# Optimization experiments

Hardware: AMD Instinct MI355X
Metric: run time of the kernel (lower is better)

## Reference

```python
import jax, jax.numpy as jnp
import numpy as np
from jax import lax

N, E, G = 20000, 640000, 16
NA, H, NG, L, NC = 21, 128, 50, 6, 97
CUTOFF = 10.0
LOG2 = 0.6931471805599453

def ssp(v):
    # ShiftedSoftplus: softplus(x) - log(2)
    return jax.nn.softplus(v) - LOG2

def setup_inputs() -> dict:
    key = jax.random.key(0)
    ks = jax.random.split(key, 24)
    s = 0.08  # xavier-ish scale for 128-wide layers
    inp = {
        "x": jax.random.normal(ks[0], (N, NA), dtype=jnp.float32),
        "pos": jax.random.uniform(ks[1], (N, 3), dtype=jnp.float32, minval=0.0, maxval=30.0),
        "edge_index": jax.random.randint(ks[2], (2, E), 0, N, dtype=jnp.int64),
        "batch": jnp.sort(jax.random.randint(ks[3], (N,), 0, G, dtype=jnp.int64)),
        # embedding Linear(21 -> 128), weights stored [in, out]
        "emb_w": jax.random.normal(ks[4], (NA, H), dtype=jnp.float32) * 0.15,
        "emb_b": jnp.zeros((H,), dtype=jnp.float32),
        # per-interaction-block params, stacked over L layers
        "mlp1_w": jax.random.normal(ks[5], (L, NG, H), dtype=jnp.float32) * 0.12,
        "mlp1_b": jnp.zeros((L, H), dtype=jnp.float32),
        "mlp2_w": jax.random.normal(ks[6], (L, H, H), dtype=jnp.float32) * s,
        "mlp2_b": jnp.zeros((L, H), dtype=jnp.float32),
        "conv1_w": jax.random.normal(ks[7], (L, H, H), dtype=jnp.float32) * s,  # no bias
        "conv2_w": jax.random.normal(ks[8], (L, H, H), dtype=jnp.float32) * s,
        "conv2_b": jnp.zeros((L, H), dtype=jnp.float32),
        "lin_w": jax.random.normal(ks[9], (L, H, H), dtype=jnp.float32) * s,
        "lin_b": jnp.zeros((L, H), dtype=jnp.float32),
        # head (note: original reuses self.lin1 twice, act is ReLU, dropout eval=identity)
        "lin1_w": jax.random.normal(ks[10], (H, H), dtype=jnp.float32) * s,
        "lin1_b": jnp.zeros((H,), dtype=jnp.float32),
        "lin2_w": jax.random.normal(ks[11], (H, NC), dtype=jnp.float32) * s,
        "lin2_b": jnp.zeros((NC,), dtype=jnp.float32),
    }
    return inp

def reference(x, pos, edge_index, batch, emb_w, emb_b, mlp1_w, mlp1_b, mlp2_w,
              mlp2_b, conv1_w, conv2_w, conv2_b, lin_w, lin_b, lin1_w, lin1_b,
              lin2_w, lin2_b):
    row, col = edge_index[0], edge_index[1]  # source j, target i
    d = pos[row] - pos[col]                  # [E,3]
    edge_weight = jnp.sqrt(jnp.sum(d * d, axis=-1))  # [E]
    # Gaussian smearing
    offset = jnp.linspace(0.0, CUTOFF, NG)
    coeff = -0.5 / (offset[1] - offset[0]) ** 2
    edge_attr = jnp.exp(coeff * (edge_weight[:, None] - offset[None, :]) ** 2)  # [E,NG]
    # cosine cutoff
    C = 0.5 * (jnp.cos(edge_weight * jnp.pi / CUTOFF) + 1.0)  # [E]

    h = x @ emb_w + emb_b  # [N,H]

    def block(h, p):
        m1w, m1b, m2w, m2b, c1w, c2w, c2b, lw, lb = p
        # edge MLP filter times cutoff envelope
        Wf = (ssp(edge_attr @ m1w + m1b) @ m2w + m2b) * C[:, None]  # [E,H]
        hx = h @ c1w                                 # lin1 (no bias)
        msg = hx[row] * Wf                           # gather + modulate
        agg = jax.ops.segment_sum(msg, col, num_segments=N)  # scatter-add
        y = ssp(agg @ c2w + c2b)
        y = y @ lw + lb
        return h + y, None

    h, _ = lax.scan(block, h, (mlp1_w, mlp1_b, mlp2_w, mlp2_b,
                               conv1_w, conv2_w, conv2_b, lin_w, lin_b))

    h = jax.nn.relu(h @ lin1_w + lin1_b)
    # global mean pool
    ones = jnp.ones((N,), dtype=h.dtype)
    counts = jnp.maximum(jax.ops.segment_sum(ones, batch, num_segments=G), 1.0)
    graph_emb = jax.ops.segment_sum(h, batch, num_segments=G) / counts[:, None]  # [G,H]
    h2 = jax.nn.relu(graph_emb @ lin1_w + lin1_b)  # lin1 reused; dropout=identity (eval)
    out = h2 @ lin2_w + lin2_b                     # [G,NC]
    return graph_emb, out
```

## Files before the change

### kernel.cpp

```cpp
#include <hip/hip_runtime.h>
#include <hip/hip_bf16.h>

#define HD 128
#define NGAUSS 50
#define NLAYER 6
#define NGRAPH 16
#define NCLS 97
#define NTAB2 8192
#define WMAX 12.0f

typedef __attribute__((ext_vector_type(8))) short bf16x8;
typedef __attribute__((ext_vector_type(4))) float f32x4;
typedef __attribute__((ext_vector_type(8))) ushort u16x8;
typedef __attribute__((ext_vector_type(4))) ushort u16x4;

__device__ __forceinline__ float ssp_f(float x) {
    float e = __expf(-fabsf(x));
    return fmaxf(x, 0.0f) + __logf(0.5f + 0.5f * e);
}
__device__ __forceinline__ ushort f2bf(float f) {
    uint u = __float_as_uint(f);
    return (ushort)((u + 0x7FFFu + ((u >> 16) & 1u)) >> 16);
}
__device__ __forceinline__ float bf2f(ushort s) {
    return __uint_as_float(((uint)s) << 16);
}

__global__ void hist_kernel(const int* __restrict__ col, int* __restrict__ deg, int E) {
    int e = blockIdx.x * blockDim.x + threadIdx.x;
    if (e < E) atomicAdd(&deg[col[e]], 1);
}

__global__ void scan1_kernel(const int* __restrict__ deg, int* __restrict__ rowp,
                             int* __restrict__ bsum, int N) {
    __shared__ int sm[256];
    const int t = threadIdx.x, i = blockIdx.x * 256 + t;
    int v = (i < N) ? deg[i] : 0;
    sm[t] = v;
    __syncthreads();
    for (int off = 1; off < 256; off <<= 1) {
        int x = sm[t];
        int a = (t >= off) ? sm[t - off] : 0;
        __syncthreads();
        sm[t] = x + a;
        __syncthreads();
    }
    if (i < N) rowp[i] = sm[t] - v;
    if (t == 255) bsum[blockIdx.x] = sm[255];
}
__global__ void scan2_kernel(const int* __restrict__ bsum, int* __restrict__ boff,
                             int NB, int* __restrict__ rowpN) {
    __shared__ int sm[256];
    const int t = threadIdx.x;
    int v = (t < NB) ? bsum[t] : 0;
    sm[t] = v;
    __syncthreads();
    for (int off = 1; off < 256; off <<= 1) {
        int x = sm[t];
        int a = (t >= off) ? sm[t - off] : 0;
        __syncthreads();
        sm[t] = x + a;
        __syncthreads();
    }
    if (t < NB) boff[t] = sm[t] - v;
    if (t == 255) *rowpN = sm[255];
}
__global__ void scan3_kernel(int* __restrict__ rowp, const int* __restrict__ boff,
                             int* __restrict__ cursor, int N) {
    int i = blockIdx.x * blockDim.x + threadIdx.x;
    if (i < N) {
        int r = rowp[i] + boff[i >> 8];
        rowp[i] = r;
        cursor[i] = r;
    }
}

__global__ void fill_kernel(const int* __restrict__ row, const int* __restrict__ col,
                            const float* __restrict__ pos, int* __restrict__ cursor,
                            uint* __restrict__ meta, int E) {
    int e = blockIdx.x * blockDim.x + threadIdx.x;
    if (e >= E) return;
    int c = col[e], r = row[e];
    int slot = atomicAdd(&cursor[c], 1);
    float dx = pos[r*3+0] - pos[c*3+0];
    float dy = pos[r*3+1] - pos[c*3+1];
    float dz = pos[r*3+2] - pos[c*3+2];
    float w = sqrtf(dx*dx + dy*dy + dz*dz);
    const float invDW = (float)(NTAB2 - 1) / WMAX;
    int i = (int)(w * invDW + 0.5f);
    i = min(i, NTAB2 - 1);
    meta[slot] = ((uint)r) | (((uint)i) << 16);
}

__global__ void prep_kernel(const float* __restrict__ m1w, const float* __restrict__ c1w,
                            const float* __restrict__ c2w, const float* __restrict__ lw,
                            const float* __restrict__ l1w, const float* __restrict__ m2w,
                            ushort* __restrict__ m1T, ushort* __restrict__ nodeThi,
                            ushort* __restrict__ nodeTlo, ushort* __restrict__ m2T) {
    int idx = blockIdx.x * blockDim.x + threadIdx.x;
    const int S1 = 6*128*64, S2 = 19*128*128, S3 = 6*128*128;
    if (idx < S1) {
        int l = idx / 8192, r = idx % 8192, c = r / 64, k = r % 64;
        float v = (k < NGAUSS) ? m1w[(size_t)l*NGAUSS*128 + k*128 + c] : 0.0f;
        m1T[(size_t)l*8192 + c*64 + k] = f2bf(v);
    } else if (idx < S1 + S2) {
        int j = idx - S1;
        int m = j / 16384, r = j % 16384, c = r / 128, k = r % 128;
        const float* src;
        if (m < 6)       src = c1w + (size_t)m*16384;
        else if (m < 12) src = c2w + (size_t)(m-6)*16384;
        else if (m < 18) src = lw  + (size_t)(m-12)*16384;
        else             src = l1w;
        float v = src[k*128 + c];
        ushort hi = f2bf(v);
        nodeThi[(size_t)m*16384 + c*128 + k] = hi;
        nodeTlo[(size_t)m*16384 + c*128 + k] = f2bf(v - bf2f(hi));
    } else if (idx < S1 + S2 + S3) {
        int j = idx - S1 - S2;
        int l = j / 16384, r = j % 16384, c = r / 128, k = r % 128;
        m2T[(size_t)l*16384 + c*128 + k] = f2bf(m2w[(size_t)l*16384 + k*128 + c]);
    }
}

__global__ void embed_kernel(const float* __restrict__ x,
                             const float* __restrict__ emb_w, const float* __restrict__ emb_b,
                             float* __restrict__ h, int N) {
    int idx = blockIdx.x * blockDim.x + threadIdx.x;
    if (idx >= N * HD) return;
    int n = idx >> 7, t = idx & 127;
    float acc = emb_b[t];
    #pragma unroll
    for (int a = 0; a < 21; ++a) acc += x[n*21 + a] * emb_w[a*HD + t];
    h[idx] = acc;
}

__global__ __launch_bounds__(256, 2) void buildtab_kernel(
        const ushort* __restrict__ m1T_all, const ushort* __restrict__ m2T_all,
        const float* __restrict__ m1b_all, const float* __restrict__ m2b_all,
        ushort* __restrict__ Tb6) {
    __shared__ ushort A1[128 * 64];
    __shared__ ushort B1[128 * 64];
    __shared__ ushort U [128 * 128];
    __shared__ float CV[128];
    char* A1b = (char*)A1;
    char* B1b = (char*)B1;
    char* Ub  = (char*)U;
    const int tid  = threadIdx.x;
    const int lane = tid & 63;
    const int wave = tid >> 6;
    const int l15  = lane & 15;
    const int kgrp = (lane >> 4) * 8;
    const int rbase = wave * 32;
    const int NTILES = NTAB2 / 128;
    const int layer = blockIdx.x / NTILES;
    const int mt    = blockIdx.x % NTILES;
    const ushort* m1T = m1T_all + (size_t)layer * 8192;
    const ushort* m2T = m2T_all + (size_t)layer * 16384;
    const float*  m1b = m1b_all + layer * HD;
    const float*  m2b = m2b_all + layer * HD;

    const float step = 10.0f / 49.0f;
    const float coeff = -0.5f / (step * step);
    const float DW = WMAX / (float)(NTAB2 - 1);

    #pragma unroll
    for (int p = 0; p < 4; ++p) {
        int rr = p * 32 + (tid >> 3);
        int k8 = (tid & 7) * 8;
        u16x8 v = *reinterpret_cast<const u16x8*>(&m1T[(size_t)rr * 64 + k8]);
        *reinterpret_cast<u16x8*>(&B1b[rr*128 + ((2*k8) ^ ((rr & 7) << 4))]) = v;
    }
    if (tid < 128) {
        float w = (float)(mt*128 + tid) * DW;
        CV[tid] = 0.5f * (__cosf(w * 0.31415926535897931f) + 1.0f);
    }

    float b1c[8], b2c[8];
    #pragma unroll
    for (int cb = 0; cb < 8; ++cb) { b1c[cb] = m1b[cb*16 + l15]; b2c[cb] = m2b[cb*16 + l15]; }

    #pragma unroll
    for (int p = 0; p < 4; ++p) {
        int rr = p * 32 + (tid >> 3);
        int k8 = (tid & 7) * 8;
        float w = (float)(mt*128 + rr) * DW;
        u16x8 v;
        #pragma unroll
        for (int j = 0; j < 8; ++j) {
            int k = k8 + j;
            float d = w - (float)k * step;
            float g = (k < NGAUSS) ? __expf(coeff * d * d) : 0.0f;
            v[j] = f2bf(g);
        }
        *reinterpret_cast<u16x8*>(&A1b[rr*128 + ((2*k8) ^ ((rr & 7) << 4))]) = v;
    }
    __syncthreads();

    f32x4 acc1[2][8];
    #pragma unroll
    for (int i = 0; i < 2; ++i)
        #pragma unroll
        for (int j = 0; j < 8; ++j) { acc1[i][j].x=0.f; acc1[i][j].y=0.f; acc1[i][j].z=0.f; acc1[i][j].w=0.f; }
    #pragma unroll
    for (int ks = 0; ks < 2; ++ks) {
        int k = ks*32 + kgrp;
        bf16x8 af[2];
        #pragma unroll
        for (int rt = 0; rt < 2; ++rt) {
            int r = rbase + rt*16 + l15;
            af[rt] = *reinterpret_cast<const bf16x8*>(&A1b[r*128 + ((2*k) ^ ((r & 7) << 4))]);
        }
        #pragma unroll
        for (int cb = 0; cb < 8; ++cb) {
            int c = cb*16 + l15;
            bf16x8 bv = *reinterpret_cast<const bf16x8*>(&B1b[c*128 + ((2*k) ^ ((c & 7) << 4))]);
            acc1[0][cb] = __builtin_amdgcn_mfma_f32_16x16x32_bf16(af[0], bv, acc1[0][cb], 0, 0, 0);
            acc1[1][cb] = __builtin_amdgcn_mfma_f32_16x16x32_bf16(af[1], bv, acc1[1][cb], 0, 0, 0);
        }
    }
    #pragma unroll
    for (int rt = 0; rt < 2; ++rt) {
        #pragma unroll
        for (int cb = 0; cb < 8; ++cb) {
            int c = cb*16 + l15;
            #pragma unroll
            for (int i = 0; i < 4; ++i) {
                int rrow = rbase + rt*16 + (lane >> 4)*4 + i;
                ushort us = f2bf(ssp_f(acc1[rt][cb][i] + b1c[cb]));
                *reinterpret_cast<ushort*>(&Ub[rrow*256 + ((2*c) ^ ((rrow & 7) << 4))]) = us;
            }
        }
    }
    __syncthreads();

    f32x4 acc2[2][8];
    #pragma unroll
    for (int i = 0; i < 2; ++i)
        #pragma unroll
        for (int j = 0; j < 8; ++j) { acc2[i][j].x=0.f; acc2[i][j].y=0.f; acc2[i][j].z=0.f; acc2[i][j].w=0.f; }
    #pragma unroll
    for (int kh = 0; kh < 2; ++kh) {
        if (kh) __syncthreads();
        #pragma unroll
        for (int p = 0; p < 4; ++p) {
            int rr = p * 32 + (tid >> 3);
            int kk = (tid & 7) * 8;
            u16x8 v = *reinterpret_cast<const u16x8*>(&m2T[(size_t)rr*128 + kh*64 + kk]);
            *reinterpret_cast<u16x8*>(&A1b[rr*128 + ((2*kk) ^ ((rr & 7) << 4))]) = v;
        }
        __syncthreads();
        #pragma unroll
        for (int ks2 = 0; ks2 < 2; ++ks2) {
            int ku = kh*64 + ks2*32 + kgrp;
            int kb = ks2*32 + kgrp;
            bf16x8 af[2];
            #pragma unroll
            for (int rt = 0; rt < 2; ++rt) {
                int r = rbase + rt*16 + l15;
                af[rt] = *reinterpret_cast<const bf16x8*>(&Ub[r*256 + ((2*ku) ^ ((r & 7) << 4))]);
            }
            #pragma unroll
            for (int cb = 0; cb < 8; ++cb) {
                int c = cb*16 + l15;
                bf16x8 bv = *reinterpret_cast<const bf16x8*>(&A1b[c*128 + ((2*kb) ^ ((c & 7) << 4))]);
                acc2[0][cb] = __builtin_amdgcn_mfma_f32_16x16x32_bf16(af[0], bv, acc2[0][cb], 0, 0, 0);
                acc2[1][cb] = __builtin_amdgcn_mfma_f32_16x16x32_bf16(af[1], bv, acc2[1][cb], 0, 0, 0);
            }
        }
    }
    __syncthreads();

    #pragma unroll
    for (int rt = 0; rt < 2; ++rt) {
        #pragma unroll
        for (int cb = 0; cb < 8; ++cb) {
            int c = cb*16 + l15;
            #pragma unroll
            for (int i = 0; i < 4; ++i) {
                int rrow = rbase + rt*16 + (lane >> 4)*4 + i;
                U[rrow*128 + c] = f2bf((acc2[rt][cb][i] + b2c[cb]) * CV[rrow]);
            }
        }
    }
    __syncthreads();
    #pragma unroll
    for (int p = 0; p < 8; ++p) {
        int idx = p * 256 + tid;
        int rr = idx >> 4;
        int k8 = (idx & 15) * 8;
        u16x8 v = *reinterpret_cast<const u16x8*>(&U[rr*128 + k8]);
        *reinterpret_cast<u16x8*>(&Tb6[((size_t)layer*NTAB2 + mt*128 + rr)*HD + k8]) = v;
    }
}

template<int EPI, bool SPLIT>
__global__ __launch_bounds__(256) void gemv64_kernel(
        const float* __restrict__ A, const ushort* __restrict__ BThi,
        const ushort* __restrict__ BTlo, const float* __restrict__ bias,
        float* __restrict__ fdst, ushort* __restrict__ bdst, int mtiles) {
    constexpr int KW   = SPLIT ? 256 : 128;
    constexpr int BROW = 2 * KW;
    __shared__ ushort Bw[128 * KW];
    __shared__ ushort A_[64 * 128];
    char* Bwb = (char*)Bw;
    char* Ab  = (char*)A_;
    const int tid  = threadIdx.x;
    const int lane = tid & 63;
    const int wave = tid >> 6;
    const int l15  = lane & 15;
    const int kgrp = (lane >> 4) * 8;
    const int rbase = wave * 16;

    if (SPLIT) {
        #pragma unroll
        for (int p = 0; p < 16; ++p) {
            int idx = p * 256 + tid;
            int c = idx >> 5;
            int k8 = (idx & 31) * 8;
            const ushort* src = (k8 < 128) ? BThi : BTlo;
            u16x8 v = *reinterpret_cast<const u16x8*>(&src[(size_t)c*128 + (k8 & 127)]);
            *reinterpret_cast<u16x8*>(&Bwb[c*BROW + ((2*k8) ^ ((c & 7) << 4))]) = v;
        }
    } else {
        #pragma unroll
        for (int p = 0; p < 8; ++p) {
            int idx = p * 256 + tid;
            int c = idx >> 4;
            int k8 = (idx & 15) * 8;
            u16x8 v = *reinterpret_cast<const u16x8*>(&BThi[(size_t)c*128 + k8]);
            *reinterpret_cast<u16x8*>(&Bwb[c*BROW + ((2*k8) ^ ((c & 7) << 4))]) = v;
        }
    }
    float bt[8];
    if (EPI == 4) {
        #pragma unroll
        for (int cb = 0; cb < 8; ++cb) bt[cb] = bias[cb*16 + l15];
    }
    __syncthreads();

    for (int mt = blockIdx.x; mt < mtiles; mt += gridDim.x) {
        #pragma unroll
        for (int p = 0; p < 8; ++p) {
            int rr = p * 8 + (tid >> 5);
            int k4 = (tid & 31) * 4;
            f32x4 v = *reinterpret_cast<const f32x4*>(&A[(size_t)(mt*64 + rr)*HD + k4]);
            u16x4 b;
            b.x = f2bf(v.x); b.y = f2bf(v.y); b.z = f2bf(v.z); b.w = f2bf(v.w);
            *reinterpret_cast<u16x4*>(&Ab[rr*256 + ((2*k4) ^ ((rr & 7) << 4))]) = b;
        }
        __syncthreads();

        bf16x8 af[4];
        {
            int r = rbase + l15;
            #pragma unroll
            for (int q = 0; q < 4; ++q)
                af[q] = *reinterpret_cast<const bf16x8*>(&Ab[r*256 + ((2*(q*32 + kgrp)) ^ ((r & 7) << 4))]);
        }
        f32x4 acc[8];
        #pragma unroll
        for (int j = 0; j < 8; ++j) { acc[j].x=0.f; acc[j].y=0.f; acc[j].z=0.f; acc[j].w=0.f; }
        #pragma unroll
        for (int ks = 0; ks < (SPLIT ? 8 : 4); ++ks) {
            int kB = ks*32 + kgrp;
            #pragma unroll
            for (int cb = 0; cb < 8; ++cb) {
                int c = cb*16 + l15;
                bf16x8 bv = *reinterpret_cast<const bf16x8*>(&Bwb[c*BROW + ((2*kB) ^ ((c & 7) << 4))]);
                acc[cb] = __builtin_amdgcn_mfma_f32_16x16x32_bf16(af[ks & 3], bv, acc[cb], 0, 0, 0);
            }
        }

        #pragma unroll
        for (int cb = 0; cb < 8; ++cb) {
            int c = cb*16 + l15;
            #pragma unroll
            for (int i = 0; i < 4; ++i) {
                int row = mt*64 + rbase + (lane >> 4)*4 + i;
                size_t off = (size_t)row * HD + c;
                if (EPI == 4) fdst[off] = fmaxf(acc[cb][i] + bt[cb], 0.0f);
                else          bdst[off] = f2bf(acc[cb][i]);
            }
        }
        __syncthreads();
    }
}

__global__ __launch_bounds__(512, 1) void nodefused_kernel(
        const ushort* __restrict__ aggb,
        const ushort* __restrict__ c2hi, const ushort* __restrict__ c2lo,
        const float* __restrict__ c2b,
        const ushort* __restrict__ lwhi, const ushort* __restrict__ lwlo,
        const float* __restrict__ lb,
        float* __restrict__ h, int mtiles) {
    __shared__ ushort W1[128 * 256];
    __shared__ ushort W2[128 * 256];
    __shared__ ushort BUF[32 * 128];
    char* W1b = (char*)W1;
    char* W2b = (char*)W2;
    char* Bu  = (char*)BUF;
    const int tid  = threadIdx.x;
    const int lane = tid & 63;
    const int wave = tid >> 6;
    const int l15  = lane & 15;
    const int kgrp = (lane >> 4) * 8;
    const int wr = (wave & 1) * 16;
    const int wc = (wave >> 1) * 2;

    #pragma unroll
    for (int p = 0; p < 8; ++p) {
        int idx = p * 512 + tid;
        int c = idx >> 5;
        int k8 = (idx & 31) * 8;
        const ushort* s1 = (k8 < 128) ? c2hi : c2lo;
        u16x8 v1 = *reinterpret_cast<const u16x8*>(&s1[(size_t)c*128 + (k8 & 127)]);
        *reinterpret_cast<u16x8*>(&W1b[c*512 + ((2*k8) ^ ((c & 7) << 4))]) = v1;
        const ushort* s2 = (k8 < 128) ? lwhi : lwlo;
        u16x8 v2 = *reinterpret_cast<const u16x8*>(&s2[(size_t)c*128 + (k8 & 127)]);
        *reinterpret_cast<u16x8*>(&W2b[c*512 + ((2*k8) ^ ((c & 7) << 4))]) = v2;
    }
    float b1c[2], b2c[2];
    #pragma unroll
    for (int cb = 0; cb < 2; ++cb) {
        int c = (wc + cb)*16 + l15;
        b1c[cb] = c2b[c];
        b2c[cb] = lb[c];
    }
    __syncthreads();

    for (int mt = blockIdx.x; mt < mtiles; mt += gridDim.x) {
        {
            int rr = tid >> 4;
            int k8 = (tid & 15) * 8;
            u16x8 v = *reinterpret_cast<const u16x8*>(&aggb[(size_t)(mt*32 + rr)*HD + k8]);
            *reinterpret_cast<u16x8*>(&Bu[rr*256 + ((2*k8) ^ ((rr & 7) << 4))]) = v;
        }
        float hp[2][4];
        #pragma unroll
        for (int cb = 0; cb < 2; ++cb) {
            int c = (wc + cb)*16 + l15;
            #pragma unroll
            for (int i = 0; i < 4; ++i) {
                int row = mt*32 + wr + (lane >> 4)*4 + i;
                hp[cb][i] = h[(size_t)row * HD + c];
            }
        }
        __syncthreads();

        bf16x8 af[4];
        {
            int r = wr + l15;
            #pragma unroll
            for (int q = 0; q < 4; ++q)
                af[q] = *reinterpret_cast<const bf16x8*>(&Bu[r*256 + ((2*(q*32 + kgrp)) ^ ((r & 7) << 4))]);
        }
        f32x4 acc[2];
        #pragma unroll
        for (int j = 0; j < 2; ++j) { acc[j].x=0.f; acc[j].y=0.f; acc[j].z=0.f; acc[j].w=0.f; }
        #pragma unroll
        for (int ks = 0; ks < 8; ++ks) {
            int kB = ks*32 + kgrp;
            #pragma unroll
            for (int cb = 0; cb < 2; ++cb) {
                int c = (wc + cb)*16 + l15;
                bf16x8 bv = *reinterpret_cast<const bf16x8*>(&W1b[c*512 + ((2*kB) ^ ((c & 7) << 4))]);
                acc[cb] = __builtin_amdgcn_mfma_f32_16x16x32_bf16(af[ks & 3], bv, acc[cb], 0, 0, 0);
            }
        }
        __syncthreads();

        #pragma unroll
        for (int cb = 0; cb < 2; ++cb) {
            int c = (wc + cb)*16 + l15;
            #pragma unroll
            for (int i = 0; i < 4; ++i) {
                int rrow = wr + (lane >> 4)*4 + i;
                ushort us = f2bf(ssp_f(acc[cb][i] + b1c[cb]));
                *reinterpret_cast<ushort*>(&Bu[rrow*256 + ((2*c) ^ ((rrow & 7) << 4))]) = us;
            }
        }
        __syncthreads();

        {
            int r = wr + l15;
            #pragma unroll
            for (int q = 0; q < 4; ++q)
                af[q] = *reinterpret_cast<const bf16x8*>(&Bu[r*256 + ((2*(q*32 + kgrp)) ^ ((r & 7) << 4))]);
        }
        #pragma unroll
        for (int j = 0; j < 2; ++j) { acc[j].x=0.f; acc[j].y=0.f; acc[j].z=0.f; acc[j].w=0.f; }
        #pragma unroll
        for (int ks = 0; ks < 8; ++ks) {
            int kB = ks*32 + kgrp;
            #pragma unroll
            for (int cb = 0; cb < 2; ++cb) {
                int c = (wc + cb)*16 + l15;
                bf16x8 bv = *reinterpret_cast<const bf16x8*>(&W2b[c*512 + ((2*kB) ^ ((c & 7) << 4))]);
                acc[cb] = __builtin_amdgcn_mfma_f32_16x16x32_bf16(af[ks & 3], bv, acc[cb], 0, 0, 0);
            }
        }
        #pragma unroll
        for (int cb = 0; cb < 2; ++cb) {
            int c = (wc + cb)*16 + l15;
            #pragma unroll
            for (int i = 0; i < 4; ++i) {
                int row = mt*32 + wr + (lane >> 4)*4 + i;
                h[(size_t)row * HD + c] = hp[cb][i] + acc[cb][i] + b2c[cb];
            }
        }
        __syncthreads();
    }
}

__global__ __launch_bounds__(256) void gathersum_kernel(
        const ushort* __restrict__ Tb, const uint* __restrict__ meta,
        const int* __restrict__ rowp, const ushort* __restrict__ hxb,
        ushort* __restrict__ aggb, int N) {
    const int lane = threadIdx.x & 63;
    const int n = blockIdx.x * 4 + (threadIdx.x >> 6);
    if (n >= N) return;
    const int c0 = lane * 2;
    const int s0 = rowp[n], s1 = rowp[n + 1];
    float al[4] = {0.f, 0.f, 0.f, 0.f};
    float ah[4] = {0.f, 0.f, 0.f, 0.f};
    int s = s0;
    for (; s + 16 <= s1; s += 16) {
        uint m[16], tv[16], hv[16];
        #pragma unroll
        for (int k = 0; k < 16; ++k) m[k] = meta[s + k];
        #pragma unroll
        for (int k = 0; k < 16; ++k) {
            tv[k] = *reinterpret_cast<const uint*>(&Tb[(size_t)(m[k] >> 16) * HD + c0]);
            hv[k] = *reinterpret_cast<const uint*>(&hxb[(size_t)(m[k] & 0xFFFFu) * HD + c0]);
        }
        #pragma unroll
        for (int k = 0; k < 16; ++k) {
            al[k & 3] += __uint_as_float(tv[k] << 16) * __uint_as_float(hv[k] << 16);
            ah[k & 3] += __uint_as_float(tv[k] & 0xFFFF0000u) * __uint_as_float(hv[k] & 0xFFFF0000u);
        }
    }
    for (; s + 4 <= s1; s += 4) {
        uint m[4], tv[4], hv[4];
        #pragma unroll
        for (int k = 0; k < 4; ++k) m[k] = meta[s + k];
        #pragma unroll
        for (int k = 0; k < 4; ++k) {
            tv[k] = *reinterpret_cast<const uint*>(&Tb[(size_t)(m[k] >> 16) * HD + c0]);
            hv[k] = *reinterpret_cast<const uint*>(&hxb[(size_t)(m[k] & 0xFFFFu) * HD + c0]);
        }
        #pragma unroll
        for (int k = 0; k < 4; ++k) {
            al[k] += __uint_as_float(tv[k] << 16) * __uint_as_float(hv[k] << 16);
            ah[k] += __uint_as_float(tv[k] & 0xFFFF0000u) * __uint_as_float(hv[k] & 0xFFFF0000u);
        }
    }
    for (; s < s1; ++s) {
        uint m0 = meta[s];
        uint tv = *reinterpret_cast<const uint*>(&Tb[(size_t)(m0 >> 16) * HD + c0]);
        uint hv = *reinterpret_cast<const uint*>(&hxb[(size_t)(m0 & 0xFFFFu) * HD + c0]);
        al[0] += __uint_as_float(tv << 16) * __uint_as_float(hv << 16);
        ah[0] += __uint_as_float(tv & 0xFFFF0000u) * __uint_as_float(hv & 0xFFFF0000u);
    }
    float lo = (al[0] + al[1]) + (al[2] + al[3]);
    float hi = (ah[0] + ah[1]) + (ah[2] + ah[3]);
    uint out = ((uint)f2bf(lo)) | (((uint)f2bf(hi)) << 16);
    *reinterpret_cast<uint*>(&aggb[(size_t)n * HD + c0]) = out;
}

__global__ void pool_kernel(const float* __restrict__ h1, const int* __restrict__ batch,
                            float* __restrict__ gsum, float* __restrict__ gcnt, int N) {
    __shared__ float pool[NGRAPH][HD];
    __shared__ float cnt[NGRAPH];
    const int t = threadIdx.x;
    #pragma unroll
    for (int g = 0; g < NGRAPH; ++g) pool[g][t] = 0.0f;
    if (t < NGRAPH) cnt[t] = 0.0f;
    __syncthreads();
    int chunk = (N + gridDim.x - 1) / gridDim.x;
    int n0 = blockIdx.x * chunk, n1 = min(N, n0 + chunk);
    for (int n = n0; n < n1; ++n) {
        int b = batch[n];
        pool[b][t] += h1[(size_t)n * HD + t];
        if (t == 0) cnt[b] += 1.0f;
    }
    __syncthreads();
    #pragma unroll
    for (int g = 0; g < NGRAPH; ++g) atomicAdd(&gsum[g*HD + t], pool[g][t]);
    if (t < NGRAPH) atomicAdd(&gcnt[t], cnt[t]);
}

__global__ void finalize_kernel(const float* __restrict__ gsum, const float* __restrict__ gcnt,
                                const float* __restrict__ l1w, const float* __restrict__ l1b,
                                const float* __restrict__ l2w, const float* __restrict__ l2b,
                                float* __restrict__ d_out) {
    __shared__ float ge[HD];
    __shared__ float h2[HD];
    const int g = blockIdx.x, t = threadIdx.x;
    float cnt = fmaxf(gcnt[g], 1.0f);
    float v = gsum[g*HD + t] / cnt;
    d_out[g*HD + t] = v;
    ge[t] = v;
    __syncthreads();
    float acc = l1b[t];
    #pragma unroll 8
    for (int k = 0; k < HD; ++k) acc += ge[k] * l1w[k*HD + t];
    h2[t] = fmaxf(acc, 0.0f);
    __syncthreads();
    if (t < NCLS) {
        float o = l2b[t];
        #pragma unroll 8
        for (int k = 0; k < HD; ++k) o += h2[k] * l2w[k*NCLS + t];
        d_out[NGRAPH*HD + g*NCLS + t] = o;
    }
}

extern "C" void kernel_launch(void* const* d_in, const int* in_sizes, int n_in,
                              void* d_out, int out_size, void* d_ws, size_t ws_size,
                              hipStream_t stream) {
    const float* x     = (const float*)d_in[0];
    const float* pos   = (const float*)d_in[1];
    const int*   eidx  = (const int*)d_in[2];
    const int*   batch = (const int*)d_in[3];
    const float* emb_w = (const float*)d_in[4];
    const float* emb_b = (const float*)d_in[5];
    const float* m1w   = (const float*)d_in[6];
    const float* m1b   = (const float*)d_in[7];
    const float* m2w   = (const float*)d_in[8];
    const float* m2b   = (const float*)d_in[9];
    const float* c1w   = (const float*)d_in[10];
    const float* c2w   = (const float*)d_in[11];
    const float* c2b   = (const float*)d_in[12];
    const float* lw    = (const float*)d_in[13];
    const float* lb    = (const float*)d_in[14];
    const float* l1w   = (const float*)d_in[15];
    const float* l1b   = (const float*)d_in[16];
    const float* l2w   = (const float*)d_in[17];
    const float* l2b   = (const float*)d_in[18];

    const int N = in_sizes[0] / 21;
    const int E = in_sizes[2] / 2;
    const int* row = eidx;
    const int* col = eidx + E;
    const int NT64 = (N + 63) / 64;
    const int NT32 = (N + 31) / 32;
    const int NB   = (N + 255) / 256;
    const int Npad = NT64 * 64 + 64;

    size_t off = 0;
    char* base = (char*)d_ws;
    auto alloc = [&](size_t bytes) -> void* {
        off = (off + 255) & ~(size_t)255;
        void* p = base + off;
        off += bytes;
        return p;
    };
    int*    deg     = (int*)alloc((size_t)N * 4);
    int*    cursor  = (int*)alloc((size_t)N * 4);
    int*    rowp    = (int*)alloc((size_t)(N + 1) * 4);
    int*    bsum    = (int*)alloc(512 * 4);
    int*    boff    = (int*)alloc(512 * 4);
    uint*   meta    = (uint*)alloc((size_t)E * 4);
    float*  h       = (float*)alloc((size_t)Npad * HD * 4);
    ushort* hxb     = (ushort*)alloc((size_t)Npad * HD * 2);
    ushort* aggb    = (ushort*)alloc((size_t)Npad * HD * 2);
    float*  h1      = (float*)alloc((size_t)Npad * HD * 4);
    ushort* Tb6     = (ushort*)alloc((size_t)6 * NTAB2 * HD * 2);
    ushort* m1T     = (ushort*)alloc((size_t)6 * 128 * 64 * 2);
    ushort* nodeThi = (ushort*)alloc((size_t)19 * 128 * 128 * 2);
    ushort* nodeTlo = (ushort*)alloc((size_t)19 * 128 * 128 * 2);
    ushort* m2T     = (ushort*)alloc((size_t)6 * 128 * 128 * 2);
    float*  gsum    = (float*)alloc((size_t)NGRAPH * HD * 4);
    float*  gcnt    = (float*)alloc((size_t)NGRAPH * 4);

    prep_kernel<<<1792, 256, 0, stream>>>(m1w, c1w, c2w, lw, l1w, m2w,
                                          m1T, nodeThi, nodeTlo, m2T);
    hipMemsetAsync(deg, 0, (size_t)N * 4, stream);
    hist_kernel<<<(E + 255)/256, 256, 0, stream>>>(col, deg, E);
    scan1_kernel<<<NB, 256, 0, stream>>>(deg, rowp, bsum, N);
    scan2_kernel<<<1, 256, 0, stream>>>(bsum, boff, NB, rowp + N);
    scan3_kernel<<<NB, 256, 0, stream>>>(rowp, boff, cursor, N);
    fill_kernel<<<(E + 255)/256, 256, 0, stream>>>(row, col, pos, cursor, meta, E);
    buildtab_kernel<<<6 * (NTAB2/128), 256, 0, stream>>>(m1T, m2T, m1b, m2b, Tb6);
    embed_kernel<<<(N*HD + 255)/256, 256, 0, stream>>>(x, emb_w, emb_b, h, N);

    gemv64_kernel<5, false><<<NT64, 256, 0, stream>>>(h, nodeThi, nullptr, nullptr,
                                                      nullptr, hxb, NT64);

    for (int l = 0; l < NLAYER; ++l) {
        const ushort* c2Thi = nodeThi + (size_t)(6 + l) * 16384;
        const ushort* c2Tlo = nodeTlo + (size_t)(6 + l) * 16384;
        const ushort* lThi  = nodeThi + (size_t)(12 + l) * 16384;
        const ushort* lTlo  = nodeTlo + (size_t)(12 + l) * 16384;

        gathersum_kernel<<<(N + 3)/4, 256, 0, stream>>>(
            Tb6 + (size_t)l * NTAB2 * HD, meta, rowp, hxb, aggb, N);

        nodefused_kernel<<<256, 512, 0, stream>>>(
            aggb, c2Thi, c2Tlo, c2b + l*HD, lThi, lTlo, lb + l*HD, h, NT32);

        if (l < NLAYER - 1) {
            gemv64_kernel<5, false><<<NT64, 256, 0, stream>>>(
                h, nodeThi + (size_t)(l + 1) * 16384, nullptr,
                nullptr, nullptr, hxb, NT64);
        } else {
            gemv64_kernel<4, true><<<NT64, 256, 0, stream>>>(
                h, nodeThi + (size_t)18 * 16384, nodeTlo + (size_t)18 * 16384,
                l1b, h1, nullptr, NT64);
        }
    }

    hipMemsetAsync(gsum, 0, (size_t)(NGRAPH*HD + NGRAPH) * 4, stream);
    pool_kernel<<<256, HD, 0, stream>>>(h1, batch, gsum, gcnt, N);
    finalize_kernel<<<NGRAPH, HD, 0, stream>>>(gsum, gcnt, l1w, l1b, l2w, l2b,
                                               (float*)d_out);
}
```

Baseline: 436.0 us.

## Fuse next-layer conv1 projection into node kernel, drop conv2 lo-split

Computes the next layer's h @ conv1_w (hx in bf16) inside nodefused_kernel right after the residual update. This removes a separate gemv64 launch and a re-read of h per layer. The conv2 weight now uses only its high bf16 part instead of the hi+lo split, which halves that GEMM's K loop and its shared-memory footprint. The cost is extra shared memory for the third weight tile and lower precision on conv2.

```diff
diff --git a/kernel.cpp b/kernel.cpp
--- a/kernel.cpp
+++ b/kernel.cpp
@@ -386,18 +386,21 @@
     }
 }
 
+template<bool CHAIN>
 __global__ __launch_bounds__(512, 1) void nodefused_kernel(
         const ushort* __restrict__ aggb,
-        const ushort* __restrict__ c2hi, const ushort* __restrict__ c2lo,
-        const float* __restrict__ c2b,
+        const ushort* __restrict__ c2T, const float* __restrict__ c2b,
         const ushort* __restrict__ lwhi, const ushort* __restrict__ lwlo,
         const float* __restrict__ lb,
-        float* __restrict__ h, int mtiles) {
-    __shared__ ushort W1[128 * 256];
+        const ushort* __restrict__ c1nT,
+        float* __restrict__ h, ushort* __restrict__ hxbn, int mtiles) {
+    __shared__ ushort W1[128 * 128];
     __shared__ ushort W2[128 * 256];
+    __shared__ ushort W3[128 * 128];
     __shared__ ushort BUF[32 * 128];
     char* W1b = (char*)W1;
     char* W2b = (char*)W2;
+    char* W3b = (char*)W3;
     char* Bu  = (char*)BUF;
     const int tid  = threadIdx.x;
     const int lane = tid & 63;
@@ -408,13 +411,22 @@
     const int wc = (wave >> 1) * 2;
 
     #pragma unroll
+    for (int p = 0; p < 4; ++p) {
+        int idx = p * 512 + tid;
+        int c = idx >> 4;
+        int k8 = (idx & 15) * 8;
+        u16x8 v1 = *reinterpret_cast<const u16x8*>(&c2T[(size_t)c*128 + k8]);
+        *reinterpret_cast<u16x8*>(&W1b[c*256 + ((2*k8) ^ ((c & 7) << 4))]) = v1;
+        if (CHAIN) {
+            u16x8 v3 = *reinterpret_cast<const u16x8*>(&c1nT[(size_t)c*128 + k8]);
+            *reinterpret_cast<u16x8*>(&W3b[c*256 + ((2*k8) ^ ((c & 7) << 4))]) = v3;
+        }
+    }
+    #pragma unroll
     for (int p = 0; p < 8; ++p) {
         int idx = p * 512 + tid;
         int c = idx >> 5;
         int k8 = (idx & 31) * 8;
-        const ushort* s1 = (k8 < 128) ? c2hi : c2lo;
-        u16x8 v1 = *reinterpret_cast<const u16x8*>(&s1[(size_t)c*128 + (k8 & 127)]);
-        *reinterpret_cast<u16x8*>(&W1b[c*512 + ((2*k8) ^ ((c & 7) << 4))]) = v1;
         const ushort* s2 = (k8 < 128) ? lwhi : lwlo;
         u16x8 v2 = *reinterpret_cast<const u16x8*>(&s2[(size_t)c*128 + (k8 & 127)]);
         *reinterpret_cast<u16x8*>(&W2b[c*512 + ((2*k8) ^ ((c & 7) << 4))]) = v2;
@@ -458,13 +470,13 @@
         #pragma unroll
         for (int j = 0; j < 2; ++j) { acc[j].x=0.f; acc[j].y=0.f; acc[j].z=0.f; acc[j].w=0.f; }
         #pragma unroll
-        for (int ks = 0; ks < 8; ++ks) {
+        for (int ks = 0; ks < 4; ++ks) {
             int kB = ks*32 + kgrp;
             #pragma unroll
             for (int cb = 0; cb < 2; ++cb) {
                 int c = (wc + cb)*16 + l15;
-                bf16x8 bv = *reinterpret_cast<const bf16x8*>(&W1b[c*512 + ((2*kB) ^ ((c & 7) << 4))]);
-                acc[cb] = __builtin_amdgcn_mfma_f32_16x16x32_bf16(af[ks & 3], bv, acc[cb], 0, 0, 0);
+                bf16x8 bv = *reinterpret_cast<const bf16x8*>(&W1b[c*256 + ((2*kB) ^ ((c & 7) << 4))]);
+                acc[cb] = __builtin_amdgcn_mfma_f32_16x16x32_bf16(af[ks], bv, acc[cb], 0, 0, 0);
             }
         }
         __syncthreads();
@@ -499,16 +511,60 @@
                 acc[cb] = __builtin_amdgcn_mfma_f32_16x16x32_bf16(af[ks & 3], bv, acc[cb], 0, 0, 0);
             }
         }
+        float hv[2][4];
         #pragma unroll
         for (int cb = 0; cb < 2; ++cb) {
             int c = (wc + cb)*16 + l15;
             #pragma unroll
             for (int i = 0; i < 4; ++i) {
                 int row = mt*32 + wr + (lane >> 4)*4 + i;
-                h[(size_t)row * HD + c] = hp[cb][i] + acc[cb][i] + b2c[cb];
-            }
-        }
-        __syncthreads();
+                hv[cb][i] = hp[cb][i] + acc[cb][i] + b2c[cb];
+                h[(size_t)row * HD + c] = hv[cb][i];
+            }
+        }
+        __syncthreads();
+
+        if (CHAIN) {
+            #pragma unroll
+            for (int cb = 0; cb < 2; ++cb) {
+                int c = (wc + cb)*16 + l15;
+                #pragma unroll
+                for (int i = 0; i < 4; ++i) {
+                    int rrow = wr + (lane >> 4)*4 + i;
+                    *reinterpret_cast<ushort*>(&Bu[rrow*256 + ((2*c) ^ ((rrow & 7) << 4))]) = f2bf(hv[cb][i]);
+                }
+            }
+            __syncthreads();
+
+            {
+                int r = wr + l15;
+                #pragma unroll
+                for (int q = 0; q < 4; ++q)
+                    af[q] = *reinterpret_cast<const bf16x8*>(&Bu[r*256 + ((2*(q*32 + kgrp)) ^ ((r & 7) << 4))]);
+            }
+            #pragma unroll
+            for (int j = 0; j < 2; ++j) { acc[j].x=0.f; acc[j].y=0.f; acc[j].z=0.f; acc[j].w=0.f; }
+            #pragma unroll
+            for (int ks = 0; ks < 4; ++ks) {
+                int kB = ks*32 + kgrp;
+                #pragma unroll
+                for (int cb = 0; cb < 2; ++cb) {
+                    int c = (wc + cb)*16 + l15;
+                    bf16x8 bv = *reinterpret_cast<const bf16x8*>(&W3b[c*256 + ((2*kB) ^ ((c & 7) << 4))]);
+                    acc[cb] = __builtin_amdgcn_mfma_f32_16x16x32_bf16(af[ks], bv, acc[cb], 0, 0, 0);
+                }
+            }
+            #pragma unroll
+            for (int cb = 0; cb < 2; ++cb) {
+                int c = (wc + cb)*16 + l15;
+                #pragma unroll
+                for (int i = 0; i < 4; ++i) {
+                    int row = mt*32 + wr + (lane >> 4)*4 + i;
+                    hxbn[(size_t)row * HD + c] = f2bf(acc[cb][i]);
+                }
+            }
+            __syncthreads();
+        }
     }
 }
 
@@ -687,22 +743,20 @@
                                                       nullptr, hxb, NT64);
 
     for (int l = 0; l < NLAYER; ++l) {
-        const ushort* c2Thi = nodeThi + (size_t)(6 + l) * 16384;
-        const ushort* c2Tlo = nodeTlo + (size_t)(6 + l) * 16384;
-        const ushort* lThi  = nodeThi + (size_t)(12 + l) * 16384;
-        const ushort* lTlo  = nodeTlo + (size_t)(12 + l) * 16384;
+        const ushort* c2T  = nodeThi + (size_t)(6 + l) * 16384;
+        const ushort* lThi = nodeThi + (size_t)(12 + l) * 16384;
+        const ushort* lTlo = nodeTlo + (size_t)(12 + l) * 16384;
 
         gathersum_kernel<<<(N + 3)/4, 256, 0, stream>>>(
             Tb6 + (size_t)l * NTAB2 * HD, meta, rowp, hxb, aggb, N);
 
-        nodefused_kernel<<<256, 512, 0, stream>>>(
-            aggb, c2Thi, c2Tlo, c2b + l*HD, lThi, lTlo, lb + l*HD, h, NT32);
-
         if (l < NLAYER - 1) {
-            gemv64_kernel<5, false><<<NT64, 256, 0, stream>>>(
-                h, nodeThi + (size_t)(l + 1) * 16384, nullptr,
-                nullptr, nullptr, hxb, NT64);
+            const ushort* c1nT = nodeThi + (size_t)(l + 1) * 16384;
+            nodefused_kernel<true><<<256, 512, 0, stream>>>(
+                aggb, c2T, c2b + l*HD, lThi, lTlo, lb + l*HD, c1nT, h, hxb, NT32);
         } else {
+            nodefused_kernel<false><<<256, 512, 0, stream>>>(
+                aggb, c2T, c2b + l*HD, lThi, lTlo, lb + l*HD, nullptr, h, nullptr, NT32);
             gemv64_kernel<4, true><<<NT64, 256, 0, stream>>>(
                 h, nodeThi + (size_t)18 * 16384, nodeTlo + (size_t)18 * 16384,
                 l1b, h1, nullptr, NT64);
```

Result: faster. 414.0 us (-5.1%).
